# Performance work log

Hardware: AMD Instinct MI355X
Metric: run time of the kernel (lower is better)

Reference implementation:

```python
import math
import jax, jax.numpy as jnp
import numpy as np

NUM_HEADS = 12
ALPHA, BETA, GAMMA = 1.9, 3.8, 15.2  # get_rpe_config(ratio=1.9)
SKIP = 1


def _rp_bucket(side):
    """iRPE euclidean contextual bucket table for a side x side grid + 1 cls token."""
    beta_int = int(BETA)
    coords = np.stack(np.meshgrid(np.arange(side), np.arange(side), indexing='ij'), -1).reshape(-1, 2)
    diff = coords[:, None, :] - coords[None, :, :]
    dis = np.round(np.sqrt((diff ** 2).sum(-1).astype(np.float64)))  # rounded euclidean distance
    far = np.clip(np.round(ALPHA + np.log(np.maximum(dis, 1e-9) / ALPHA) / math.log(GAMMA / ALPHA) * (BETA - ALPHA)), None, BETA)
    idx = np.where(dis <= ALPHA, dis, far).astype(np.int32) + beta_int
    num_buckets = 2 * beta_int + 1  # 7
    L = side * side
    full = np.full((L + SKIP, L + SKIP), num_buckets, dtype=np.int32)  # extra bucket for cls
    full[SKIP:, SKIP:] = idx
    return full, num_buckets + 1  # table [P,P], total buckets = 8


def setup_inputs() -> dict:
    key = jax.random.key(0)
    ks = jax.random.split(key, 8)
    B, P, n_mod, C = 64, 197, 2, 768
    N = 1 + (P - 1) * n_mod  # 393
    hd = C // NUM_HEADS
    rp_bucket, n_buckets = _rp_bucket(int(math.sqrt(P - SKIP)))
    s = 0.02
    return {
        'x': jax.random.normal(ks[0], (B, N, C), jnp.float32),
        'q_learned': jax.random.normal(ks[1], (1, 1, C), jnp.float32) * s,
        'pos_embed': jax.random.normal(ks[2], (1, P, C), jnp.float32) * s,
        'wk': jax.random.normal(ks[3], (C, C), jnp.float32) * s,
        'wv': jax.random.normal(ks[4], (C, C), jnp.float32) * s,
        'rpe_w': jax.random.normal(ks[5], (hd, n_buckets), jnp.float32) * s,  # shared_head ctx lookup table
        'proj_w': jax.random.normal(ks[6], (C, C), jnp.float32) * s,
        'proj_b': jnp.zeros((C,), jnp.float32),
        'rp_bucket': jnp.asarray(rp_bucket),  # [P, P] int32
    }


def reference(x, q_learned, pos_embed, wk, wv, rpe_w, proj_w, proj_b, rp_bucket):
    B, N, C = x.shape
    H = NUM_HEADS
    hd = C // H
    P = rp_bucket.shape[0]
    n_mod = (N - 1) // (P - 1)
    scale = hd ** -0.5

    q_ = jnp.broadcast_to(q_learned + pos_embed, (B, P, C))
    q = q_.reshape(B, P, H, hd).transpose(0, 2, 1, 3)                    # bhpd
    k = (x @ wk.T).reshape(B, N, H, hd).transpose(0, 2, 1, 3)            # bhnd
    v = (x @ wv.T).reshape(B, N, H, hd).transpose(0, 2, 1, 3)            # bhnd

    attn = jnp.einsum('bhpd,bhnd->bhpn', q, k) * scale                   # [B,H,P,N]

    # contextual RPE on keys: lookup = q @ table, gathered by rp_bucket[i, j]
    lookup = jnp.einsum('bhpd,du->bhpu', q, rpe_w)                        # [B,H,P,n_buckets]
    bias = lookup[:, :, jnp.arange(P)[:, None], rp_bucket]                # [B,H,P,P]
    bias = jnp.concatenate([bias[..., :1], jnp.tile(bias[..., 1:], (1, 1, 1, n_mod))], axis=-1)
    attn = jax.nn.softmax(attn + bias, axis=-1)

    out = jnp.einsum('bhpn,bhnd->bhpd', attn, v).transpose(0, 2, 1, 3).reshape(B, P, C)
    return out @ proj_w.T + proj_b
```

## Files before the change

kernel.cpp:

```cpp
#include <hip/hip_runtime.h>

typedef unsigned short u16;
typedef short bf16x8 __attribute__((ext_vector_type(8)));
typedef float f32x4 __attribute__((ext_vector_type(4)));
typedef const __attribute__((address_space(1))) void* gptr_t;
typedef __attribute__((address_space(3))) void* lptr_t;

#define B_   64
#define N_   393
#define C_   768
#define H_   12
#define HD_  64
#define P_   197
#define BIAS_N 416
#define PPAD 208
#define VTP  448
#define M_KV (B_ * N_)
#define M_PR (B_ * P_)
#define SCALE_L2E 0.180336879f

__device__ __forceinline__ u16 f2bf(float f) {
    unsigned u = __float_as_uint(f);
    return (u16)((u + 0x7FFFu + ((u >> 16) & 1u)) >> 16);
}
__device__ __forceinline__ unsigned cvt_pk_bf16(float lo, float hi) {
    unsigned r;
    asm("v_cvt_pk_bf16_f32 %0, %1, %2" : "=v"(r) : "v"(lo), "v"(hi));
    return r;
}
__device__ __forceinline__ float exp2_fast(float x) {
    float r;
    asm("v_exp_f32 %0, %1" : "=v"(r) : "v"(x));
    return r;
}

__global__ __launch_bounds__(256) void conv_all(
    const float* __restrict__ x, const float* __restrict__ wk,
    const float* __restrict__ wv, const float* __restrict__ pw,
    u16* __restrict__ xh, u16* __restrict__ wkvh, u16* __restrict__ pwh)
{
    const int XN4 = 19316736 / 4;
    const int WN4 = 589824 / 4;
    int i = blockIdx.x * 256 + threadIdx.x;
    const float* src; u16* dst; int off;
    if (i < XN4) { src = x; dst = xh; off = i; }
    else {
        int j = i - XN4;
        int sec = j / WN4;
        off = j - sec * WN4;
        src = sec == 0 ? wk : (sec == 1 ? wv : pw);
        dst = sec == 0 ? wkvh : (sec == 1 ? wkvh + 589824 : pwh);
    }
    float4 v = ((const float4*)src)[off];
    u16 o[4] = {f2bf(v.x), f2bf(v.y), f2bf(v.z), f2bf(v.w)};
    *(uint2*)(dst + off * 4) = *(uint2*)o;
}

__global__ __launch_bounds__(256) void prep1_kernel(
    const float* __restrict__ q_learned, const float* __restrict__ pos_embed,
    const float* __restrict__ rpe_w, u16* __restrict__ qh, float* __restrict__ lk)
{
    __shared__ float q_s[C_];
    const int p = blockIdx.x, t = threadIdx.x;
    for (int c = t; c < C_; c += 256) {
        float v = q_learned[c] + pos_embed[p * C_ + c];
        q_s[c] = v;
        qh[p * C_ + c] = f2bf(v);
    }
    __syncthreads();
    if (t < H_ * 8) {
        int h = t >> 3, u = t & 7;
        float s = 0.f;
        #pragma unroll 8
        for (int d = 0; d < HD_; ++d)
            s = fmaf(q_s[h * HD_ + d], rpe_w[d * 8 + u], s);
        lk[(h * P_ + p) * 8 + u] = s;
    }
}

__global__ __launch_bounds__(256) void prep2_kernel(
    const float* __restrict__ lk, const int* __restrict__ rp_bucket,
    float* __restrict__ biasT)
{
    int bx = blockIdx.x;
    int h = bx / N_, j = bx % N_;
    int t = threadIdx.x;
    if (t >= PPAD) return;
    int jm;
    if (j == 0) jm = 0;
    else { jm = j - 1; if (jm >= 196) jm -= 196; jm += 1; }
    float v = 0.f;
    if (t < P_) {
        int bucket = rp_bucket[t * P_ + jm];
        v = lk[(h * P_ + t) * 8 + bucket] * 1.44269504f;
    }
    biasT[((size_t)h * BIAS_N + j) * PPAD + t] = v;
}

template <bool F32OUT>
__global__ __launch_bounds__(256) void gemm_bf16(
    const u16* __restrict__ A, const u16* __restrict__ Bw,
    u16* __restrict__ Cb, float* __restrict__ Cf, const float* __restrict__ bias,
    int M, int ldc)
{
    __shared__ __align__(16) u16 As[128 * 64];
    __shared__ __align__(16) u16 Bs[128 * 64];

    const int gx = gridDim.x;
    const int nwg = gx * gridDim.y;
    const int orig = blockIdx.y * gx + blockIdx.x;
    const int xcd = orig & 7, rank = orig >> 3;
    const int q = nwg >> 3, r = nwg & 7;
    const int wgid = (xcd < r ? xcd * (q + 1) : r * (q + 1) + (xcd - r) * q) + rank;
    const int n0 = (wgid % gx) * 128;
    const int m0 = (wgid / gx) * 128;

    const int t = threadIdx.x;
    const int w = t >> 6, l = t & 63;
    const int wr = w >> 1, wc = w & 1;
    const int l15 = l & 15, lg = l >> 4;
    const int lrow = l >> 3, lslot = l & 7;
    const int Mc = M - 1;

    f32x4 acc[4][4];
    #pragma unroll
    for (int i = 0; i < 4; ++i)
        #pragma unroll
        for (int j = 0; j < 4; ++j) acc[i][j] = (f32x4){0.f, 0.f, 0.f, 0.f};

    for (int ks = 0; ks < 12; ++ks) {
        const int k0 = ks * 64;
        if (ks) __syncthreads();
        #pragma unroll
        for (int i = 0; i < 4; ++i) {
            const int rbase = w * 32 + i * 8;
            int arow = m0 + rbase + lrow; if (arow > Mc) arow = Mc;
            const int brow = n0 + rbase + lrow;
            const u16* ga = A  + (size_t)arow * 768 + k0 + lslot * 8;
            const u16* gb = Bw + (size_t)brow * 768 + k0 + lslot * 8;
            __builtin_amdgcn_global_load_lds((gptr_t)(const void*)ga,
                                             (lptr_t)(void*)(As + rbase * 64), 16, 0, 0);
            __builtin_amdgcn_global_load_lds((gptr_t)(const void*)gb,
                                             (lptr_t)(void*)(Bs + rbase * 64), 16, 0, 0);
        }
        __syncthreads();
        #pragma unroll
        for (int kk = 0; kk < 2; ++kk) {
            bf16x8 af[4], bfr[4];
            #pragma unroll
            for (int mf = 0; mf < 4; ++mf) {
                af[mf]  = *(const bf16x8*)(As + (wr * 64 + mf * 16 + l15) * 64 + (kk * 4 + lg) * 8);
                bfr[mf] = *(const bf16x8*)(Bs + (wc * 64 + mf * 16 + l15) * 64 + (kk * 4 + lg) * 8);
            }
            #pragma unroll
            for (int mf = 0; mf < 4; ++mf)
                #pragma unroll
                for (int nf = 0; nf < 4; ++nf)
                    acc[mf][nf] = __builtin_amdgcn_mfma_f32_16x16x32_bf16(
                        af[mf], bfr[nf], acc[mf][nf], 0, 0, 0);
        }
    }

    #pragma unroll
    for (int mf = 0; mf < 4; ++mf) {
        #pragma unroll
        for (int nf = 0; nf < 4; ++nf) {
            int col = n0 + wc * 64 + nf * 16 + l15;
            float bb = 0.f;
            if (F32OUT) bb = bias[col];
            #pragma unroll
            for (int rr = 0; rr < 4; ++rr) {
                int m = m0 + wr * 64 + mf * 16 + lg * 4 + rr;
                if (m < M) {
                    if (F32OUT) Cf[(size_t)m * ldc + col] = acc[mf][nf][rr] + bb;
                    else        Cb[(size_t)m * ldc + col] = f2bf(acc[mf][nf][rr]);
                }
            }
        }
    }
}

__global__ __launch_bounds__(256) void vtrans_kernel(const u16* __restrict__ KV,
                                                     u16* __restrict__ Vt)
{
    const int bh = blockIdx.x;
    const int b = bh / H_, h = bh % H_;
    const int t = threadIdx.x, w = t >> 6, l = t & 63;
    const int d = w * 16 + (l >> 2);
    const int c = l & 3;
    const u16* src = KV + (size_t)b * N_ * 1536 + 768 + h * HD_ + d;
    u16* dst = Vt + (size_t)(bh * HD_ + d) * VTP;
    for (int jb = 0; jb < VTP; jb += 32) {
        int j0 = jb + c * 8;
        u16 v[8];
        #pragma unroll
        for (int i = 0; i < 8; ++i) {
            int j = j0 + i;
            v[i] = (j < N_) ? src[(size_t)j * 1536] : (u16)0;
        }
        *(bf16x8*)(dst + j0) = *(bf16x8*)v;
    }
}

__global__ __launch_bounds__(256, 2) void attn_mfma4(
    const u16* __restrict__ qh, const u16* __restrict__ KV,
    const u16* __restrict__ Vt, const float* __restrict__ biasT,
    u16* __restrict__ Obuf)
{
    __shared__ __align__(16) u16 pts[64 * 456];
    __shared__ __align__(16) u16 kvs[2][64 * 64];

    const int id = blockIdx.x;
    const int work = (id & 7) * 384 + (id >> 3);
    const int ptile = work & 3;
    const int rest = work >> 2;
    const int h = rest % 12;
    const int b = rest / 12;
    const int p0 = ptile * 64;

    const int t = threadIdx.x, w = t >> 6, l = t & 63;
    const int l15 = l & 15, lg = l >> 4;
    const int p0w = p0 + w * 16;

    int srow[2], sslot[2], swoff[2];
    #pragma unroll
    for (int i = 0; i < 2; ++i) {
        int c = t + 256 * i;
        srow[i] = c >> 3; sslot[i] = c & 7;
        swoff[i] = srow[i] * 64 + ((sslot[i] ^ (srow[i] & 7)) << 3);
    }

    int prow = p0w + l15; if (prow > P_ - 1) prow = P_ - 1;
    const u16* qp = qh + (size_t)prow * C_ + h * HD_ + lg * 8;
    bf16x8 qf0 = *(const bf16x8*)(qp);
    bf16x8 qf1 = *(const bf16x8*)(qp + 32);

    const u16* Kbase = KV + (size_t)b * (N_ * 1536) + h * HD_;
    const u16* Vbase = Vt + (size_t)(b * H_ + h) * (HD_ * VTP);

    f32x4 acc[7][4];
    #pragma unroll
    for (int i = 0; i < 7; ++i)
        #pragma unroll
        for (int j = 0; j < 4; ++j) acc[i][j] = (f32x4){0.f, 0.f, 0.f, 0.f};

    bf16x8 ra[2];
    #pragma unroll
    for (int i = 0; i < 2; ++i)
        ra[i] = *(const bf16x8*)(Kbase + (size_t)srow[i] * 1536 + sslot[i] * 8);
    #pragma unroll
    for (int i = 0; i < 2; ++i) *(bf16x8*)(&kvs[0][swoff[i]]) = ra[i];
    __syncthreads();

    #pragma unroll
    for (int nt = 0; nt < 7; ++nt) {
        const u16* kcur = kvs[nt & 1];
        if (nt < 6) {
            #pragma unroll
            for (int i = 0; i < 2; ++i) {
                int rn = (nt + 1) * 64 + srow[i]; if (rn > N_ - 1) rn = N_ - 1;
                ra[i] = *(const bf16x8*)(Kbase + (size_t)rn * 1536 + sslot[i] * 8);
            }
        }
        __builtin_amdgcn_s_setprio(1);
        #pragma unroll
        for (int kc = 0; kc < 2; ++kc)
            #pragma unroll
            for (int sub = 0; sub < 4; ++sub) {
                int row = sub * 16 + l15;
                bf16x8 kb = *(const bf16x8*)(kcur + row * 64 + (((kc * 4 + lg) ^ (row & 7)) << 3));
                acc[nt][sub] = __builtin_amdgcn_mfma_f32_16x16x32_bf16(
                    kc ? qf1 : qf0, kb, acc[nt][sub], 0, 0, 0);
            }
        __builtin_amdgcn_s_setprio(0);
        if (nt < 6) {
            #pragma unroll
            for (int i = 0; i < 2; ++i) *(bf16x8*)(&kvs[(nt + 1) & 1][swoff[i]]) = ra[i];
        }
        __syncthreads();
    }

    #pragma unroll
    for (int i = 0; i < 2; ++i)
        ra[i] = *(const bf16x8*)(Vbase + (size_t)srow[i] * VTP + sslot[i] * 8);

    const int pcl = (p0w + lg * 4) > (PPAD - 4) ? (PPAD - 4) : (p0w + lg * 4);
    float s4[4] = {0.f, 0.f, 0.f, 0.f};
    #pragma unroll
    for (int nt = 0; nt < 7; ++nt)
        #pragma unroll
        for (int sub = 0; sub < 4; ++sub) {
            int n = nt * 64 + sub * 16 + l15;
            if (n < N_) {
                float4 b4 = *(const float4*)(biasT + ((size_t)h * BIAS_N + n) * PPAD + pcl);
                float bb[4] = {b4.x, b4.y, b4.z, b4.w};
                #pragma unroll
                for (int rr = 0; rr < 4; ++rr) {
                    float e = exp2_fast(fmaf(acc[nt][sub][rr], SCALE_L2E, bb[rr]));
                    acc[nt][sub][rr] = e;
                    s4[rr] += e;
                }
            } else {
                acc[nt][sub] = (f32x4){0.f, 0.f, 0.f, 0.f};
            }
        }
    float rinv4[4];
    #pragma unroll
    for (int rr = 0; rr < 4; ++rr) {
        float s = s4[rr];
        s += __shfl_xor(s, 1); s += __shfl_xor(s, 2);
        s += __shfl_xor(s, 4); s += __shfl_xor(s, 8);
        rinv4[rr] = 1.0f / s;
    }

    {
        const int rowb = w * 16 + lg * 4;
        #pragma unroll
        for (int nt = 0; nt < 7; ++nt)
            #pragma unroll
            for (int sub = 0; sub < 4; ++sub) {
                int col = nt * 64 + sub * 16 + l15;
                unsigned pk01 = cvt_pk_bf16(acc[nt][sub][0], acc[nt][sub][1]);
                unsigned pk23 = cvt_pk_bf16(acc[nt][sub][2], acc[nt][sub][3]);
                pts[(rowb + 0) * 456 + col] = (u16)pk01;
                pts[(rowb + 1) * 456 + col] = (u16)(pk01 >> 16);
                pts[(rowb + 2) * 456 + col] = (u16)pk23;
                pts[(rowb + 3) * 456 + col] = (u16)(pk23 >> 16);
            }
    }
    #pragma unroll
    for (int i = 0; i < 2; ++i) *(bf16x8*)(&kvs[0][swoff[i]]) = ra[i];
    __syncthreads();

    f32x4 o[4];
    #pragma unroll
    for (int i = 0; i < 4; ++i) o[i] = (f32x4){0.f, 0.f, 0.f, 0.f};

    #pragma unroll
    for (int nt = 0; nt < 7; ++nt) {
        const u16* kcur = kvs[nt & 1];
        if (nt < 6) {
            #pragma unroll
            for (int i = 0; i < 2; ++i)
                ra[i] = *(const bf16x8*)(Vbase + (size_t)srow[i] * VTP + (nt + 1) * 64 + sslot[i] * 8);
        }
        __builtin_amdgcn_s_setprio(1);
        #pragma unroll
        for (int kc = 0; kc < 2; ++kc) {
            bf16x8 pa = *(const bf16x8*)(pts + (w * 16 + l15) * 456 + nt * 64 + kc * 32 + lg * 8);
            #pragma unroll
            for (int dsub = 0; dsub < 4; ++dsub) {
                int row = dsub * 16 + l15;
                bf16x8 vb = *(const bf16x8*)(kcur + row * 64 + (((kc * 4 + lg) ^ (row & 7)) << 3));
                o[dsub] = __builtin_amdgcn_mfma_f32_16x16x32_bf16(pa, vb, o[dsub], 0, 0, 0);
            }
        }
        __builtin_amdgcn_s_setprio(0);
        if (nt < 6) {
            #pragma unroll
            for (int i = 0; i < 2; ++i) *(bf16x8*)(&kvs[(nt + 1) & 1][swoff[i]]) = ra[i];
        }
        __syncthreads();
    }

    #pragma unroll
    for (int dsub = 0; dsub < 4; ++dsub)
        #pragma unroll
        for (int rr = 0; rr < 4; ++rr) {
            int p = p0w + lg * 4 + rr;
            if (p < P_)
                Obuf[((size_t)b * P_ + p) * C_ + h * HD_ + dsub * 16 + l15] =
                    f2bf(o[dsub][rr] * rinv4[rr]);
        }
}

extern "C" void kernel_launch(void* const* d_in, const int* in_sizes, int n_in,
                              void* d_out, int out_size, void* d_ws, size_t ws_size,
                              hipStream_t stream)
{
    const float* x         = (const float*)d_in[0];
    const float* q_learned = (const float*)d_in[1];
    const float* pos_embed = (const float*)d_in[2];
    const float* wk        = (const float*)d_in[3];
    const float* wv        = (const float*)d_in[4];
    const float* rpe_w     = (const float*)d_in[5];
    const float* proj_w    = (const float*)d_in[6];
    const float* proj_b    = (const float*)d_in[7];
    const int*   rp_bucket = (const int*)d_in[8];
    float* out = (float*)d_out;

    char* ws = (char*)d_ws;
    u16*   xh    = (u16*)(ws);
    u16*   wkvh  = (u16*)(ws + 38633472);
    u16*   pwh   = (u16*)(ws + 40992768);
    u16*   qh    = (u16*)(ws + 42172416);
    float* lk    = (float*)(ws + 42475008);
    float* biasT = (float*)(ws + 42550784);
    u16*   KV    = (u16*)(ws + 46704128);
    u16*   Vt    = (u16*)(ws + 123971072);
    u16*   Obuf  = (u16*)(ws + 168011264);

    conv_all<<<20592, 256, 0, stream>>>(x, wk, wv, proj_w, xh, wkvh, pwh);

    prep1_kernel<<<P_, 256, 0, stream>>>(q_learned, pos_embed, rpe_w, qh, lk);
    prep2_kernel<<<H_ * N_, 256, 0, stream>>>(lk, rp_bucket, biasT);

    dim3 gkv(1536 / 128, (M_KV + 127) / 128);
    gemm_bf16<false><<<gkv, 256, 0, stream>>>(xh, wkvh, KV, nullptr, nullptr, M_KV, 1536);

    vtrans_kernel<<<B_ * H_, 256, 0, stream>>>(KV, Vt);

    attn_mfma4<<<3072, 256, 0, stream>>>(qh, KV, Vt, biasT, Obuf);

    dim3 gpr(768 / 128, (M_PR + 127) / 128);
    gemm_bf16<true><<<gpr, 256, 0, stream>>>(Obuf, pwh, nullptr, out, proj_b, M_PR, 768);
}
```

Measured before the change: 239.2 us.

## Replace KV GEMM with 256x256 tiled 8-wave pipelined kernel; trim attention tail tile

The K/V projection GEMM moves to a new 512-thread kernel with 256x256 tiles and a 64K-element LDS ring buffer. It uses swizzled layouts and an explicit schedule of async global-to-LDS loads paired with s_waitcnt and barriers, so memory traffic overlaps MFMA work. The attention kernel now skips the fully padded key sub-tiles in the last 64-wide chunk, in both QK and PV, and zeroes the affected P columns so no garbage is read. The risks are one workgroup per CU from the large LDS footprint, and a fragile hand-written vmcnt schedule.

Result: slower. 249.5 us (+4.3%).

```diff
diff --git a/kernel.cpp b/kernel.cpp
--- a/kernel.cpp
+++ b/kernel.cpp
@@ -97,11 +97,144 @@
     biasT[((size_t)h * BIAS_N + j) * PPAD + t] = v;
 }
 
-template <bool F32OUT>
-__global__ __launch_bounds__(256) void gemm_bf16(
+__global__ __launch_bounds__(512, 1) void gemm_kv8(
+    const u16* __restrict__ A, const u16* __restrict__ Bw, u16* __restrict__ KV)
+{
+    __shared__ __align__(16) u16 lds[65536];
+
+    const int nwg = 6 * 99;
+    const int orig = blockIdx.y * 6 + blockIdx.x;
+    const int xcd = orig & 7, rank = orig >> 3;
+    const int q = nwg >> 3, r = nwg & 7;
+    const int wgid = (xcd < r ? xcd * (q + 1) : r * (q + 1) + (xcd - r) * q) + rank;
+    const int n0 = (wgid % 6) * 256;
+    const int m0 = (wgid / 6) * 256;
+
+    const int t = threadIdx.x;
+    const int wid = t >> 6, l = t & 63;
+    const int wr = wid >> 2, wc = wid & 3;
+    const int l15 = l & 15, lg = l >> 4;
+    const int Mc = M_KV - 1;
+
+    const u16* gA[2]; const u16* gB[2];
+    #pragma unroll
+    for (int i = 0; i < 2; ++i) {
+        int c = t + 512 * i;
+        int prow = c >> 2, s = c & 3;
+        int row = prow ^ ((prow >> 2) & 1);
+        int slot = s ^ (row & 3);
+        int arow = m0 + row; if (arow > Mc) arow = Mc;
+        gA[i] = A + (size_t)arow * 768 + slot * 8;
+        gB[i] = Bw + (size_t)(n0 + row) * 768 + slot * 8;
+    }
+
+    int au[8], bu[4];
+    #pragma unroll
+    for (int mf = 0; mf < 8; ++mf) {
+        int rowu = wr * 128 + mf * 16 + l15;
+        au[mf] = ((rowu ^ ((rowu >> 2) & 1)) * 4 + (lg ^ (rowu & 3))) * 8;
+    }
+    #pragma unroll
+    for (int nf = 0; nf < 4; ++nf) {
+        int colu = wc * 64 + nf * 16 + l15;
+        bu[nf] = ((colu ^ ((colu >> 2) & 1)) * 4 + (lg ^ (colu & 3))) * 8;
+    }
+
+    f32x4 acc[8][4];
+    #pragma unroll
+    for (int i = 0; i < 8; ++i)
+        #pragma unroll
+        for (int j = 0; j < 4; ++j) acc[i][j] = (f32x4){0.f, 0.f, 0.f, 0.f};
+
+#define STAGE_UNIT(XSEL, KT, KAP) do {                                          \
+    unsigned _lb = ((XSEL) ? 32768u : 0u) +                                     \
+                   (unsigned)(((((KT) & 1) * 2 + (KAP)) * 8192));               \
+    const u16* _g0 = (XSEL) ? gB[0] : gA[0];                                    \
+    const u16* _g1 = (XSEL) ? gB[1] : gA[1];                                    \
+    __builtin_amdgcn_global_load_lds((gptr_t)(const void*)(_g0 + (KT)*64 + (KAP)*32), \
+        (lptr_t)(void*)(lds + _lb + (unsigned)t * 8), 16, 0, 0);                \
+    __builtin_amdgcn_global_load_lds((gptr_t)(const void*)(_g1 + (KT)*64 + (KAP)*32), \
+        (lptr_t)(void*)(lds + _lb + (unsigned)(t + 512) * 8), 16, 0, 0);        \
+} while (0)
+
+#define QPHASE(KT, Q, VMLIT, DOSTG, SX, SKT, SKAP) do {                         \
+    const int _db = (KT) & 1;                                                   \
+    const int _kap = (Q) >> 1;                                                  \
+    const int _mh = (Q) & 1;                                                    \
+    const unsigned _ab = (unsigned)((_db * 2 + _kap) * 8192);                   \
+    const unsigned _bb = 32768u + _ab;                                          \
+    bf16x8 _af[4], _bf[4];                                                      \
+    _Pragma("unroll") for (int _j = 0; _j < 4; ++_j) {                          \
+        _af[_j] = *(const bf16x8*)(lds + _ab + au[_mh * 4 + _j]);               \
+        _bf[_j] = *(const bf16x8*)(lds + _bb + bu[_j]); }                       \
+    if (DOSTG) STAGE_UNIT(SX, SKT, SKAP);                                       \
+    asm volatile("s_waitcnt vmcnt(" #VMLIT ")" ::: "memory");                   \
+    __builtin_amdgcn_s_barrier();                                               \
+    asm volatile("s_waitcnt lgkmcnt(0)" ::: "memory");                          \
+    __builtin_amdgcn_sched_barrier(0);                                          \
+    __builtin_amdgcn_s_setprio(1);                                              \
+    _Pragma("unroll") for (int _j = 0; _j < 4; ++_j)                            \
+        _Pragma("unroll") for (int _nf = 0; _nf < 4; ++_nf)                     \
+            acc[_mh * 4 + _j][_nf] = __builtin_amdgcn_mfma_f32_16x16x32_bf16(   \
+                _af[_j], _bf[_nf], acc[_mh * 4 + _j][_nf], 0, 0, 0);            \
+    __builtin_amdgcn_s_setprio(0);                                              \
+    __builtin_amdgcn_s_barrier();                                               \
+} while (0)
+
+    STAGE_UNIT(0, 0, 0); STAGE_UNIT(1, 0, 0);
+    STAGE_UNIT(0, 0, 1); STAGE_UNIT(1, 0, 1);
+    STAGE_UNIT(0, 1, 0); STAGE_UNIT(1, 1, 0);
+    STAGE_UNIT(0, 1, 1); STAGE_UNIT(1, 1, 1);
+    asm volatile("s_waitcnt vmcnt(12)" ::: "memory");
+    __builtin_amdgcn_s_barrier();
+
+    QPHASE(0, 0, 12, 0, 0, 0, 0);
+    QPHASE(0, 1, 8,  0, 0, 0, 0);
+    QPHASE(0, 2, 8,  1, 0, 2, 0);
+    QPHASE(0, 3, 8,  1, 1, 2, 0);
+    QPHASE(1, 0, 8,  1, 0, 2, 1);
+    QPHASE(1, 1, 8,  1, 1, 2, 1);
+    QPHASE(1, 2, 8,  1, 0, 3, 0);
+    QPHASE(1, 3, 8,  1, 1, 3, 0);
+    for (int it = 1; it <= 4; ++it) {
+        const int kt0 = 2 * it, kt1 = 2 * it + 1;
+        QPHASE(kt0, 0, 8, 1, 0, kt1,     1);
+        QPHASE(kt0, 1, 8, 1, 1, kt1,     1);
+        QPHASE(kt0, 2, 8, 1, 0, kt0 + 2, 0);
+        QPHASE(kt0, 3, 8, 1, 1, kt0 + 2, 0);
+        QPHASE(kt1, 0, 8, 1, 0, kt0 + 2, 1);
+        QPHASE(kt1, 1, 8, 1, 1, kt0 + 2, 1);
+        QPHASE(kt1, 2, 8, 1, 0, kt1 + 2, 0);
+        QPHASE(kt1, 3, 8, 1, 1, kt1 + 2, 0);
+    }
+    QPHASE(10, 0, 8, 1, 0, 11, 1);
+    QPHASE(10, 1, 8, 1, 1, 11, 1);
+    QPHASE(10, 2, 6, 0, 0, 0, 0);
+    QPHASE(10, 3, 4, 0, 0, 0, 0);
+    QPHASE(11, 0, 2, 0, 0, 0, 0);
+    QPHASE(11, 1, 0, 0, 0, 0, 0);
+    QPHASE(11, 2, 0, 0, 0, 0, 0);
+    QPHASE(11, 3, 0, 0, 0, 0, 0);
+
+#undef QPHASE
+#undef STAGE_UNIT
+
+    #pragma unroll
+    for (int mf = 0; mf < 8; ++mf)
+        #pragma unroll
+        for (int nf = 0; nf < 4; ++nf) {
+            int col = n0 + wc * 64 + nf * 16 + l15;
+            #pragma unroll
+            for (int rr = 0; rr < 4; ++rr) {
+                int m = m0 + wr * 128 + mf * 16 + lg * 4 + rr;
+                if (m < M_KV) KV[(size_t)m * 1536 + col] = f2bf(acc[mf][nf][rr]);
+            }
+        }
+}
+
+__global__ __launch_bounds__(256) void gemm_proj(
     const u16* __restrict__ A, const u16* __restrict__ Bw,
-    u16* __restrict__ Cb, float* __restrict__ Cf, const float* __restrict__ bias,
-    int M, int ldc)
+    float* __restrict__ Cf, const float* __restrict__ bias)
 {
     __shared__ __align__(16) u16 As[128 * 64];
     __shared__ __align__(16) u16 Bs[128 * 64];
@@ -120,7 +253,7 @@
     const int wr = w >> 1, wc = w & 1;
     const int l15 = l & 15, lg = l >> 4;
     const int lrow = l >> 3, lslot = l & 7;
-    const int Mc = M - 1;
+    const int Mc = M_PR - 1;
 
     f32x4 acc[4][4];
     #pragma unroll
@@ -162,22 +295,17 @@
     }
 
     #pragma unroll
-    for (int mf = 0; mf < 4; ++mf) {
+    for (int mf = 0; mf < 4; ++mf)
         #pragma unroll
         for (int nf = 0; nf < 4; ++nf) {
             int col = n0 + wc * 64 + nf * 16 + l15;
-            float bb = 0.f;
-            if (F32OUT) bb = bias[col];
+            float bb = bias[col];
             #pragma unroll
             for (int rr = 0; rr < 4; ++rr) {
                 int m = m0 + wr * 64 + mf * 16 + lg * 4 + rr;
-                if (m < M) {
-                    if (F32OUT) Cf[(size_t)m * ldc + col] = acc[mf][nf][rr] + bb;
-                    else        Cb[(size_t)m * ldc + col] = f2bf(acc[mf][nf][rr]);
-                }
-            }
-        }
-    }
+                if (m < M_PR) Cf[(size_t)m * 768 + col] = acc[mf][nf][rr] + bb;
+            }
+        }
 }
 
 __global__ __launch_bounds__(256) void vtrans_kernel(const u16* __restrict__ KV,
@@ -202,7 +330,7 @@
     }
 }
 
-__global__ __launch_bounds__(256, 2) void attn_mfma4(
+__global__ __launch_bounds__(256, 2) void attn_mfma5(
     const u16* __restrict__ qh, const u16* __restrict__ KV,
     const u16* __restrict__ Vt, const float* __restrict__ biasT,
     u16* __restrict__ Obuf)
@@ -262,11 +390,12 @@
                 ra[i] = *(const bf16x8*)(Kbase + (size_t)rn * 1536 + sslot[i] * 8);
             }
         }
+        const int smax = (nt == 6) ? 1 : 4;
         __builtin_amdgcn_s_setprio(1);
         #pragma unroll
         for (int kc = 0; kc < 2; ++kc)
             #pragma unroll
-            for (int sub = 0; sub < 4; ++sub) {
+            for (int sub = 0; sub < smax; ++sub) {
                 int row = sub * 16 + l15;
                 bf16x8 kb = *(const bf16x8*)(kcur + row * 64 + (((kc * 4 + lg) ^ (row & 7)) << 3));
                 acc[nt][sub] = __builtin_amdgcn_mfma_f32_16x16x32_bf16(
@@ -287,9 +416,10 @@
     const int pcl = (p0w + lg * 4) > (PPAD - 4) ? (PPAD - 4) : (p0w + lg * 4);
     float s4[4] = {0.f, 0.f, 0.f, 0.f};
     #pragma unroll
-    for (int nt = 0; nt < 7; ++nt)
-        #pragma unroll
-        for (int sub = 0; sub < 4; ++sub) {
+    for (int nt = 0; nt < 7; ++nt) {
+        const int smax = (nt == 6) ? 1 : 4;
+        #pragma unroll
+        for (int sub = 0; sub < smax; ++sub) {
             int n = nt * 64 + sub * 16 + l15;
             if (n < N_) {
                 float4 b4 = *(const float4*)(biasT + ((size_t)h * BIAS_N + n) * PPAD + pcl);
@@ -304,6 +434,7 @@
                 acc[nt][sub] = (f32x4){0.f, 0.f, 0.f, 0.f};
             }
         }
+    }
     float rinv4[4];
     #pragma unroll
     for (int rr = 0; rr < 4; ++rr) {
@@ -316,9 +447,10 @@
     {
         const int rowb = w * 16 + lg * 4;
         #pragma unroll
-        for (int nt = 0; nt < 7; ++nt)
-            #pragma unroll
-            for (int sub = 0; sub < 4; ++sub) {
+        for (int nt = 0; nt < 7; ++nt) {
+            const int smax = (nt == 6) ? 1 : 4;
+            #pragma unroll
+            for (int sub = 0; sub < smax; ++sub) {
                 int col = nt * 64 + sub * 16 + l15;
                 unsigned pk01 = cvt_pk_bf16(acc[nt][sub][0], acc[nt][sub][1]);
                 unsigned pk23 = cvt_pk_bf16(acc[nt][sub][2], acc[nt][sub][3]);
@@ -327,6 +459,10 @@
                 pts[(rowb + 2) * 456 + col] = (u16)pk23;
                 pts[(rowb + 3) * 456 + col] = (u16)(pk23 >> 16);
             }
+        }
+        #pragma unroll
+        for (int rr = 0; rr < 4; ++rr)
+            pts[(rowb + rr) * 456 + 400 + l15] = 0;
     }
     #pragma unroll
     for (int i = 0; i < 2; ++i) *(bf16x8*)(&kvs[0][swoff[i]]) = ra[i];
@@ -344,9 +480,10 @@
             for (int i = 0; i < 2; ++i)
                 ra[i] = *(const bf16x8*)(Vbase + (size_t)srow[i] * VTP + (nt + 1) * 64 + sslot[i] * 8);
         }
+        const int kcmax = (nt == 6) ? 1 : 2;
         __builtin_amdgcn_s_setprio(1);
         #pragma unroll
-        for (int kc = 0; kc < 2; ++kc) {
+        for (int kc = 0; kc < kcmax; ++kc) {
             bf16x8 pa = *(const bf16x8*)(pts + (w * 16 + l15) * 456 + nt * 64 + kc * 32 + lg * 8);
             #pragma unroll
             for (int dsub = 0; dsub < 4; ++dsub) {
@@ -405,13 +542,13 @@
     prep1_kernel<<<P_, 256, 0, stream>>>(q_learned, pos_embed, rpe_w, qh, lk);
     prep2_kernel<<<H_ * N_, 256, 0, stream>>>(lk, rp_bucket, biasT);
 
-    dim3 gkv(1536 / 128, (M_KV + 127) / 128);
-    gemm_bf16<false><<<gkv, 256, 0, stream>>>(xh, wkvh, KV, nullptr, nullptr, M_KV, 1536);
+    dim3 gkv(6, 99);
+    gemm_kv8<<<gkv, 512, 0, stream>>>(xh, wkvh, KV);
 
     vtrans_kernel<<<B_ * H_, 256, 0, stream>>>(KV, Vt);
 
-    attn_mfma4<<<3072, 256, 0, stream>>>(qh, KV, Vt, biasT, Obuf);
+    attn_mfma5<<<3072, 256, 0, stream>>>(qh, KV, Vt, biasT, Obuf);
 
     dim3 gpr(768 / 128, (M_PR + 127) / 128);
-    gemm_bf16<true><<<gpr, 256, 0, stream>>>(Obuf, pwh, nullptr, out, proj_b, M_PR, 768);
-}
+    gemm_proj<<<gpr, 256, 0, stream>>>(Obuf, pwh, out, proj_b);
+}
```
